# Kernel tuning notes

Hardware: AMD Instinct MI355X
Metric: run time of the kernel (lower is better)

## Reference

```python
import jax, jax.numpy as jnp
import numpy as np

E = 128       # embed_dim
H = 128       # hidden_dim
NLABEL = 5
VOCAB = 50000
DEPTH = 18    # levels 0..17, complete binary tree
BRANCH = 2
N_NODES = 2 ** DEPTH - 1  # level-order layout: level l occupies [2^l-1, 2^(l+1)-1)


def setup_inputs() -> dict:
    key = jax.random.key(0)
    ks = jax.random.split(key, 24)

    def w(k, shape):
        return jax.random.normal(k, shape, dtype=jnp.float32) * 0.05

    inp = {
        "embeds": w(ks[0], (VOCAB, E)),
        "node_words": jax.random.randint(ks[1], (N_NODES,), 0, VOCAB),
        "node_labels": jax.random.randint(ks[2], (N_NODES,), 0, NLABEL),
        "depth": DEPTH,
        "branching": BRANCH,
    }
    # 8 gate linears: *x maps E->H, *h maps H->H (torch nn.Linear: y = x @ W.T + b)
    for j, nm in enumerate(["ix", "ih", "fx", "fh", "ox", "oh", "ux", "uh"]):
        in_dim = E if nm.endswith("x") else H
        inp["W" + nm] = w(ks[3 + 2 * j], (H, in_dim))
        inp["b" + nm] = w(ks[4 + 2 * j], (H,))
    inp["Wout"] = w(ks[20], (NLABEL, H))
    inp["bout"] = w(ks[21], (NLABEL,))
    return inp


def _lin(x, W, b):
    return x @ W.T + b


def _tree_lstm(embeds, node_words, node_labels, depth, branching,
               Wix, bix, Wih, bih, Wfx, bfx, Wfh, bfh,
               Wox, box, Woh, boh, Wux, bux, Wuh, buh, Wout, bout):
    b = branching
    hid = Wix.shape[0]
    loss = jnp.zeros((), dtype=embeds.dtype)
    child_c = child_h = None
    logp = None
    # bottom-up over levels (leaves first); level l has b^l nodes at offset (b^l-1)/(b-1)
    for l in range(depth - 1, -1, -1):
        n = b ** l
        off = (b ** l - 1) // (b - 1)
        x = embeds[node_words[off:off + n]]            # [n, E]
        if child_h is None:                            # leaves: zero child states
            h_sum = jnp.zeros((n, hid), dtype=embeds.dtype)
            c_agg = jnp.zeros((n, hid), dtype=embeds.dtype)
        else:
            ch = child_h.reshape(n, b, hid)            # children of each level-l node
            cc = child_c.reshape(n, b, hid)
            h_sum = ch.sum(axis=1)                     # child-sum
            f = jax.nn.sigmoid(_lin(x, Wfx, bfx)[:, None, :] + _lin(ch, Wfh, bfh))
            c_agg = (f * cc).sum(axis=1)               # sum_k f_k * c_k
        i = jax.nn.sigmoid(_lin(x, Wix, bix) + _lin(h_sum, Wih, bih))
        o = jax.nn.sigmoid(_lin(x, Wox, box) + _lin(h_sum, Woh, boh))
        u = jnp.tanh(_lin(x, Wux, bux) + _lin(h_sum, Wuh, buh))
        c = i * u + c_agg
        h = o * jnp.tanh(c)
        logp = jax.nn.log_softmax(_lin(h, Wout, bout), axis=-1)   # [n, NLABEL]
        lab = node_labels[off:off + n]
        loss = loss - logp[jnp.arange(n), lab].sum()              # NLL summed over nodes
        child_c, child_h = c, h
    return logp, loss  # logp from level 0 = root log-probs [1, NLABEL]


def reference(embeds, node_words, node_labels, depth, branching,
              Wix, bix, Wih, bih, Wfx, bfx, Wfh, bfh,
              Wox, box, Woh, boh, Wux, bux, Wuh, buh, Wout, bout):
    return _tree_lstm(embeds, node_words, node_labels, depth, branching,
                      Wix, bix, Wih, bih, Wfx, bfx, Wfh, bfh,
                      Wox, box, Woh, boh, Wux, bux, Wuh, buh, Wout, bout)
```

## Files before the change

### kernel.cpp

```cpp
#include <hip/hip_runtime.h>
#include <math.h>

#define DEPTH 18
#define NINT ((1 << (DEPTH - 1)) - 1)
#define LEAF_OFF ((1 << (DEPTH - 2)) - 1)
#define NVOCAB 50000
#define SAW 520
#define KTS 9

typedef unsigned short bf16raw;
typedef __bf16 bf16x8 __attribute__((ext_vector_type(8)));
typedef float f32x4 __attribute__((ext_vector_type(4)));
typedef short short8 __attribute__((ext_vector_type(8)));

__device__ __forceinline__ float sigm(float x) { return 1.0f / (1.0f + __expf(-x)); }
__device__ __forceinline__ float fast_tanh(float x) {
    float t = __expf(2.0f * x);
    return 1.0f - 2.0f / (t + 1.0f);
}

__device__ __forceinline__ float bf2f(bf16raw u) {
    union { unsigned int i; float f; } v;
    v.i = ((unsigned int)u) << 16;
    return v.f;
}
__device__ __forceinline__ bf16raw f2bf(float f) {
    union { float f; unsigned int i; } v;
    v.f = f;
    unsigned int r = v.i + 0x7FFFu + ((v.i >> 16) & 1u);
    return (bf16raw)(r >> 16);
}

#define SB() __builtin_amdgcn_sched_barrier(0)

__global__ __launch_bounds__(256) void k_prep_embeds(const float* __restrict__ src,
                                                     bf16raw* __restrict__ dst, int n4)
{
    int i = blockIdx.x * blockDim.x + threadIdx.x;
    if (i < n4) {
        float4 v = ((const float4*)src)[i];
        ushort4 o;
        o.x = f2bf(v.x); o.y = f2bf(v.y); o.z = f2bf(v.z); o.w = f2bf(v.w);
        ((ushort4*)dst)[i] = o;
    }
}

__global__ __launch_bounds__(128) void k_prep_bcat(
    const float* __restrict__ Wix, const float* __restrict__ bix,
    const float* __restrict__ Wih, const float* __restrict__ bih,
    const float* __restrict__ Wfx, const float* __restrict__ bfx,
    const float* __restrict__ Wfh, const float* __restrict__ bfh,
    const float* __restrict__ Wox, const float* __restrict__ box_,
    const float* __restrict__ Woh, const float* __restrict__ boh,
    const float* __restrict__ Wux, const float* __restrict__ bux,
    const float* __restrict__ Wuh, const float* __restrict__ buh,
    bf16raw* __restrict__ Bfrag, float* __restrict__ bias_cat)
{
    const int j = blockIdx.x;
    const int gate = j >> 7, jj = j & 127;
    const float *Wx, *Wh, *bx, *bh;
    switch (gate) {
        case 0: Wx = Wix; Wh = Wih; bx = bix;  bh = bih; break;
        case 1: Wx = Wux; Wh = Wuh; bx = bux;  bh = buh; break;
        case 2: Wx = Wox; Wh = Woh; bx = box_; bh = boh; break;
        default: Wx = Wfx; Wh = Wfh; bx = bfx; bh = bfh; break;
    }
    const int coltile = (j >> 4) & 7, lr = j & 15;
    for (int k = threadIdx.x; k < 256; k += blockDim.x) {
        float v = (k < 128) ? Wx[jj * 128 + k] : Wh[jj * 128 + (k - 128)];
        const int idx = (((gate * 8 + coltile) * KTS + (k >> 5)) * 64
                         + ((k >> 3) & 3) * 16 + lr) * 8 + (k & 7);
        Bfrag[idx] = f2bf(v);
    }
    if (threadIdx.x == 0) bias_cat[j] = bx[jj] + bh[jj];
}

template<int CB>
__device__ __forceinline__ void lp_burst(const bf16raw* __restrict__ bfbase, int wcol,
                                         bf16x8 (&bb)[16])
{
#pragma unroll
    for (int kt = 0; kt < 4; ++kt)
#pragma unroll
        for (int j = 0; j < 4; ++j)
            bb[kt * 4 + j] = *(const bf16x8*)(bfbase +
                    (long)(((CB * 8 + (wcol >> 4) + j) * KTS + kt) * 512));
}

__device__ __forceinline__ void lp_mfma_all(const bf16raw* __restrict__ sA, int wrow,
                                            int lrow, int lquad,
                                            bf16x8 (&bb)[16], f32x4 (&acc)[2][4])
{
#pragma unroll
    for (int kt = 0; kt < 4; ++kt) {
        bf16x8 af[2];
#pragma unroll
        for (int i = 0; i < 2; ++i)
            af[i] = *(const bf16x8*)&sA[(wrow + i * 16 + lrow) * 136 + kt * 32 + lquad * 8];
#pragma unroll
        for (int i = 0; i < 2; ++i)
#pragma unroll
            for (int j = 0; j < 4; ++j)
                acc[i][j] = __builtin_amdgcn_mfma_f32_16x16x32_bf16(af[i], bb[kt * 4 + j], acc[i][j], 0, 0, 0);
    }
}

template<int CB>
__device__ __forceinline__ void lp_rungemm(const bf16raw* __restrict__ sA,
                                           const bf16raw* __restrict__ bfbase,
                                           int wrow, int wcol, int lrow, int lquad,
                                           f32x4 (&acc)[2][4])
{
#pragma unroll
    for (int i = 0; i < 2; i++)
#pragma unroll
        for (int j = 0; j < 4; j++) acc[i][j] = (f32x4){0.f, 0.f, 0.f, 0.f};
    bf16x8 bb[16];
    lp_burst<CB>(bfbase, wcol, bb);
    SB();
    lp_mfma_all(sA, wrow, lrow, lquad, bb, acc);
}

template<int G, int H>
__device__ __forceinline__ void load8(const bf16raw* __restrict__ bfbase, int w,
                                      bf16x8 (&bb)[8])
{
#pragma unroll
    for (int kt2 = 0; kt2 < 4; ++kt2)
#pragma unroll
        for (int jj = 0; jj < 2; ++jj)
            bb[kt2 * 2 + jj] = *(const bf16x8*)(bfbase +
                    (long)(((G * 8 + w * 2 + jj) * KTS + H * 4 + kt2) * 512));
}

template<int AB>
__device__ __forceinline__ void mfma4k(const bf16raw* __restrict__ sA, int lrow, int lquad,
                                       bf16x8 (&bb)[8], f32x4 (&acc)[2][2])
{
#pragma unroll
    for (int kt2 = 0; kt2 < 4; ++kt2) {
        bf16x8 af[2];
#pragma unroll
        for (int i = 0; i < 2; ++i)
            af[i] = *(const bf16x8*)&sA[(i * 16 + lrow) * SAW + (AB + kt2) * 32 + lquad * 8];
#pragma unroll
        for (int jj = 0; jj < 2; ++jj)
#pragma unroll
            for (int i = 0; i < 2; ++i)
                acc[i][jj] = __builtin_amdgcn_mfma_f32_16x16x32_bf16(af[i], bb[kt2 * 2 + jj], acc[i][jj], 0, 0, 0);
    }
}

__global__ __launch_bounds__(256, 3) void k_leafpre(
    const bf16raw* __restrict__ embeds_bf,
    const bf16raw* __restrict__ Bfrag, const float* __restrict__ bias_cat,
    const float* __restrict__ Wout, const float* __restrict__ bout,
    bf16raw* __restrict__ hc_leaf, float* __restrict__ lossv6, int nvtot)
{
    const int vbase = blockIdx.x * 64;
    int nv = nvtot - vbase;
    if (nv > 64) nv = 64;
    if (nv <= 0) return;

    __shared__ __align__(16) bf16raw sA[64 * 136];
    __shared__ __align__(16) bf16raw sT[64 * 136];
    __shared__ float sWout[5 * 128];

    const int t = threadIdx.x;
    for (int i = t; i < 640; i += 256) sWout[i] = Wout[i];

    {
        const int row = t >> 2;
        const int co = (t & 3) * 32;
        const int arow = (row < nv) ? row : 0;
        const bf16raw* ax = embeds_bf + (long)(vbase + arow) * 128;
        *(short8*)&sA[row * 136 + co]      = *(const short8*)(ax + co);
        *(short8*)&sA[row * 136 + co + 8]  = *(const short8*)(ax + co + 8);
        *(short8*)&sA[row * 136 + co + 16] = *(const short8*)(ax + co + 16);
        *(short8*)&sA[row * 136 + co + 24] = *(const short8*)(ax + co + 24);
    }

    const int lane = t & 63;
    const int w = t >> 6;
    const int wrow = (w & 1) * 32;
    const int wcol = (w >> 1) * 64;
    const int lrow = lane & 15;
    const int lquad = lane >> 4;

    __syncthreads();

    const bf16raw* bfbase = Bfrag + (long)lane * 8;

    float tval[2][4][4];
    f32x4 acc[2][4];

    lp_rungemm<0>(sA, bfbase, wrow, wcol, lrow, lquad, acc);
#pragma unroll
    for (int i = 0; i < 2; i++)
#pragma unroll
        for (int jj = 0; jj < 4; jj++) {
            const float b = bias_cat[wcol + jj * 16 + lrow];
#pragma unroll
            for (int r = 0; r < 4; r++) tval[i][jj][r] = sigm(acc[i][jj][r] + b);
        }
    lp_rungemm<1>(sA, bfbase, wrow, wcol, lrow, lquad, acc);
#pragma unroll
    for (int i = 0; i < 2; i++)
#pragma unroll
        for (int jj = 0; jj < 4; jj++) {
            const float b = bias_cat[128 + wcol + jj * 16 + lrow];
#pragma unroll
            for (int r = 0; r < 4; r++) tval[i][jj][r] *= fast_tanh(acc[i][jj][r] + b);
        }
#pragma unroll
    for (int i = 0; i < 2; i++)
#pragma unroll
        for (int jj = 0; jj < 4; jj++)
#pragma unroll
            for (int r = 0; r < 4; r++) {
                const int m = wrow + i * 16 + lquad * 4 + r;
                const int j = wcol + jj * 16 + lrow;
                sT[m * 136 + j] = f2bf(tval[i][jj][r]);
            }
#pragma unroll
    for (int i = 0; i < 2; i++)
#pragma unroll
        for (int jj = 0; jj < 4; jj++)
#pragma unroll
            for (int r = 0; r < 4; r++) tval[i][jj][r] = fast_tanh(tval[i][jj][r]);
    __syncthreads();
#pragma unroll
    for (int s = 0; s < 4; ++s) {
        int ci = t + 256 * s;
        int row = ci >> 4, c8 = (ci & 15) * 8;
        if (row < nv)
            *(short8*)(hc_leaf + (long)(vbase + row) * 256 + 128 + c8) = *(const short8*)&sT[row * 136 + c8];
    }
    lp_rungemm<2>(sA, bfbase, wrow, wcol, lrow, lquad, acc);
    __syncthreads();
#pragma unroll
    for (int i = 0; i < 2; i++)
#pragma unroll
        for (int jj = 0; jj < 4; jj++) {
            const float b = bias_cat[256 + wcol + jj * 16 + lrow];
#pragma unroll
            for (int r = 0; r < 4; r++) {
                const int m = wrow + i * 16 + lquad * 4 + r;
                const int j = wcol + jj * 16 + lrow;
                sT[m * 136 + j] = f2bf(sigm(acc[i][jj][r] + b) * tval[i][jj][r]);
            }
        }
    __syncthreads();
#pragma unroll
    for (int s = 0; s < 4; ++s) {
        int ci = t + 256 * s;
        int row = ci >> 4, c8 = (ci & 15) * 8;
        if (row < nv)
            *(short8*)(hc_leaf + (long)(vbase + row) * 256 + c8) = *(const short8*)&sT[row * 136 + c8];
    }
    {
        const int row = t >> 2, q = t & 3;
        float p[5] = {0.f, 0.f, 0.f, 0.f, 0.f};
        for (int k0 = 0; k0 < 32; ++k0) {
            const int k = q * 32 + k0;
            float hv = bf2f(sT[row * 136 + k]);
#pragma unroll
            for (int l = 0; l < 5; l++) p[l] += hv * sWout[l * 128 + k];
        }
#pragma unroll
        for (int l = 0; l < 5; l++) {
            p[l] += __shfl_down(p[l], 2);
            p[l] += __shfl_down(p[l], 1);
        }
        if (q == 0 && row < nv) {
            float lg[5], mx = -1e30f;
#pragma unroll
            for (int l = 0; l < 5; l++) {
                lg[l] = p[l] + bout[l];
                mx = fmaxf(mx, lg[l]);
            }
            float se = 0.f;
#pragma unroll
            for (int l = 0; l < 5; l++) se += __expf(lg[l] - mx);
            float lse = __logf(se) + mx;
            float* dst = lossv6 + (long)(vbase + row) * 6;
#pragma unroll
            for (int l = 0; l < 5; l++) dst[l] = lg[l];
            dst[5] = lse;
        }
    }
}

__global__ __launch_bounds__(256, 3) void k_level32(
    const bf16raw* __restrict__ embeds_bf, const int* __restrict__ words,
    bf16raw* __restrict__ h_all, bf16raw* __restrict__ c_all,
    const bf16raw* __restrict__ hc_leaf,
    const bf16raw* __restrict__ Bfrag, const float* __restrict__ bias_cat,
    int off, int nm, int leafkids)
{
    __shared__ __align__(16) bf16raw sA[32 * SAW];
    __shared__ __align__(16) bf16raw sCT[64 * 136];

    const int t = threadIdx.x;
    const int m0 = blockIdx.x * 32;

    {
        const int row = t >> 3;
        const int co = (t & 7) * 8;
        int mm = m0 + row; if (mm >= nm) mm = nm - 1;
        const long g = (long)off + mm;
        const bf16raw* px = embeds_bf + (long)words[g] * 128;
        const bf16raw *p1, *p2;
        if (leafkids) {
            p1 = hc_leaf + (long)words[2 * g + 1] * 256;
            p2 = hc_leaf + (long)words[2 * g + 2] * 256;
        } else {
            p1 = h_all + (2 * g + 1) * 128;
            p2 = h_all + (2 * g + 2) * 128;
        }
        short8 vx0 = *(const short8*)(px + co);
        short8 vx1 = *(const short8*)(px + 64 + co);
        short8 h10 = *(const short8*)(p1 + co);
        short8 h11 = *(const short8*)(p1 + 64 + co);
        short8 h20 = *(const short8*)(p2 + co);
        short8 h21 = *(const short8*)(p2 + 64 + co);
        short8 hs0, hs1;
#pragma unroll
        for (int e = 0; e < 8; ++e) {
            hs0[e] = (short)f2bf(bf2f((bf16raw)(unsigned short)h10[e]) +
                                 bf2f((bf16raw)(unsigned short)h20[e]));
            hs1[e] = (short)f2bf(bf2f((bf16raw)(unsigned short)h11[e]) +
                                 bf2f((bf16raw)(unsigned short)h21[e]));
        }
        *(short8*)&sA[row * SAW + co]        = vx0;
        *(short8*)&sA[row * SAW + 64 + co]   = vx1;
        *(short8*)&sA[row * SAW + 128 + co]  = hs0;
        *(short8*)&sA[row * SAW + 192 + co]  = hs1;
        *(short8*)&sA[row * SAW + 256 + co]  = h10;
        *(short8*)&sA[row * SAW + 320 + co]  = h11;
        *(short8*)&sA[row * SAW + 384 + co]  = h20;
        *(short8*)&sA[row * SAW + 448 + co]  = h21;
    }
    {
        const int slot = t >> 2;
        const int cc8 = (t & 3) * 8;
        int mm = m0 + (slot >> 1); if (mm >= nm) mm = nm - 1;
        const long g = (long)off + mm;
        const long cg = 2 * g + 1 + (slot & 1);
        const bf16raw* pc = leafkids ? (hc_leaf + (long)words[cg] * 256 + 128)
                                     : (c_all + cg * 128);
#pragma unroll
        for (int s = 0; s < 4; ++s)
            *(short8*)&sCT[slot * 136 + s * 32 + cc8] = *(const short8*)(pc + s * 32 + cc8);
    }

    const int lane = t & 63;
    const int w = t >> 6;
    const int lrow = lane & 15;
    const int lquad = lane >> 4;

    float bias[4][2];
#pragma unroll
    for (int g = 0; g < 4; ++g)
#pragma unroll
        for (int jj = 0; jj < 2; ++jj)
            bias[g][jj] = bias_cat[g * 128 + w * 32 + jj * 16 + lrow];

    __syncthreads();

    const bf16raw* bfbase = Bfrag + (long)lane * 8;

    f32x4 acc[2][2];
    f32x4 fx[2][2];
    float si[2][2][4];
    float cc[2][2][4];
    float hh[2][2][4];
    bf16x8 bbA[8], bbB[8];

#define ZACC() { _Pragma("unroll") for (int i_ = 0; i_ < 2; ++i_) \
                 _Pragma("unroll") for (int j_ = 0; j_ < 2; ++j_) \
                     acc[i_][j_] = (f32x4){0.f, 0.f, 0.f, 0.f}; }

    load8<0, 0>(bfbase, w, bbA);
    load8<0, 1>(bfbase, w, bbB);
    SB();
    ZACC();
    mfma4k<0>(sA, lrow, lquad, bbA, acc); SB();
    load8<1, 0>(bfbase, w, bbA); SB();
    mfma4k<4>(sA, lrow, lquad, bbB, acc); SB();
    load8<1, 1>(bfbase, w, bbB); SB();
#pragma unroll
    for (int i = 0; i < 2; ++i)
#pragma unroll
        for (int jj = 0; jj < 2; ++jj)
#pragma unroll
            for (int r = 0; r < 4; ++r)
                si[i][jj][r] = sigm(acc[i][jj][r] + bias[0][jj]);
    ZACC();
    mfma4k<0>(sA, lrow, lquad, bbA, acc); SB();
    load8<3, 0>(bfbase, w, bbA); SB();
    mfma4k<4>(sA, lrow, lquad, bbB, acc); SB();
    load8<3, 1>(bfbase, w, bbB); SB();
#pragma unroll
    for (int i = 0; i < 2; ++i)
#pragma unroll
        for (int jj = 0; jj < 2; ++jj)
#pragma unroll
            for (int r = 0; r < 4; ++r)
                cc[i][jj][r] = si[i][jj][r] * fast_tanh(acc[i][jj][r] + bias[1][jj]);
    ZACC();
    mfma4k<0>(sA, lrow, lquad, bbA, acc);
    SB();
#pragma unroll
    for (int i = 0; i < 2; ++i)
#pragma unroll
        for (int jj = 0; jj < 2; ++jj) fx[i][jj] = acc[i][jj];
    mfma4k<8>(sA, lrow, lquad, bbB, acc);
    SB();
    load8<2, 0>(bfbase, w, bbA);
    SB();
#pragma unroll
    for (int i = 0; i < 2; ++i)
#pragma unroll
        for (int jj = 0; jj < 2; ++jj) {
            const int j = w * 32 + jj * 16 + lrow;
#pragma unroll
            for (int r = 0; r < 4; ++r) {
                const int m = i * 16 + lquad * 4 + r;
                cc[i][jj][r] += sigm(acc[i][jj][r] + bias[3][jj]) * bf2f(sCT[(2 * m) * 136 + j]);
            }
        }
#pragma unroll
    for (int i = 0; i < 2; ++i)
#pragma unroll
        for (int jj = 0; jj < 2; ++jj) acc[i][jj] = fx[i][jj];
    mfma4k<12>(sA, lrow, lquad, bbB, acc);
    SB();
    load8<2, 1>(bfbase, w, bbB);
    SB();
#pragma unroll
    for (int i = 0; i < 2; ++i)
#pragma unroll
        for (int jj = 0; jj < 2; ++jj) {
            const int j = w * 32 + jj * 16 + lrow;
#pragma unroll
            for (int r = 0; r < 4; ++r) {
                const int m = i * 16 + lquad * 4 + r;
                cc[i][jj][r] += sigm(acc[i][jj][r] + bias[3][jj]) * bf2f(sCT[(2 * m + 1) * 136 + j]);
            }
        }
    ZACC();
    mfma4k<0>(sA, lrow, lquad, bbA, acc);
    mfma4k<4>(sA, lrow, lquad, bbB, acc);
    SB();
#pragma unroll
    for (int i = 0; i < 2; ++i)
#pragma unroll
        for (int jj = 0; jj < 2; ++jj)
#pragma unroll
            for (int r = 0; r < 4; ++r)
                hh[i][jj][r] = sigm(acc[i][jj][r] + bias[2][jj]) * fast_tanh(cc[i][jj][r]);
#undef ZACC

    __syncthreads();

#pragma unroll
    for (int i = 0; i < 2; ++i)
#pragma unroll
        for (int jj = 0; jj < 2; ++jj) {
            const int j = w * 32 + jj * 16 + lrow;
#pragma unroll
            for (int r = 0; r < 4; ++r) {
                const int m = i * 16 + lquad * 4 + r;
                sCT[m * 136 + j] = f2bf(cc[i][jj][r]);
                sCT[(32 + m) * 136 + j] = f2bf(hh[i][jj][r]);
            }
        }
    __syncthreads();

#pragma unroll
    for (int q = 0; q < 4; ++q) {
        int ci = t + 256 * q;
        int row = ci >> 4;
        int c8 = (ci & 15) * 8;
        int m = row & 31;
        if (m0 + m < nm) {
            bf16raw* dst = (row < 32) ? c_all : h_all;
            *(short8*)(dst + ((long)off + m0 + m) * 128 + c8) = *(const short8*)&sCT[row * 136 + c8];
        }
    }
}

__global__ __launch_bounds__(256) void k_loss(
    const bf16raw* __restrict__ h_all, const int* __restrict__ words,
    const int* __restrict__ labels, const float* __restrict__ lossv6,
    const float* __restrict__ Wout, const float* __restrict__ bout,
    float* __restrict__ partials, float* __restrict__ out)
{
    __shared__ float sWout[640];
    __shared__ float red[128];
    const int t = threadIdx.x;
    for (int i = t; i < 640; i += 256) sWout[i] = Wout[i];

    const int row = t >> 1, half = t & 1;
    const long g = (long)blockIdx.x * 128 + row;
    const bool valid = g < NINT;
    const long gg = valid ? g : 0;
    __syncthreads();

    float p[5] = {0.f, 0.f, 0.f, 0.f, 0.f};
    const bf16raw* hp = h_all + gg * 128 + half * 64;
#pragma unroll
    for (int s = 0; s < 8; ++s) {
        short8 v = *(const short8*)(hp + s * 8);
#pragma unroll
        for (int e = 0; e < 8; ++e) {
            float hv = bf2f((bf16raw)(unsigned short)v[e]);
#pragma unroll
            for (int l = 0; l < 5; l++) p[l] += hv * sWout[l * 128 + half * 64 + s * 8 + e];
        }
    }
#pragma unroll
    for (int l = 0; l < 5; l++) p[l] += __shfl_down(p[l], 1);

    float lossNode = 0.f;
    if (half == 0 && valid) {
        float lg[5], mx = -1e30f;
#pragma unroll
        for (int l = 0; l < 5; l++) {
            lg[l] = p[l] + bout[l];
            mx = fmaxf(mx, lg[l]);
        }
        float se = 0.f;
#pragma unroll
        for (int l = 0; l < 5; l++) se += __expf(lg[l] - mx);
        float lse = __logf(se) + mx;
        lossNode = lse - lg[labels[gg]];
        if (gg >= LEAF_OFF) {
            const float* lv1 = lossv6 + (long)words[2 * gg + 1] * 6;
            const float* lv2 = lossv6 + (long)words[2 * gg + 2] * 6;
            lossNode += (lv1[5] - lv1[labels[2 * gg + 1]])
                      + (lv2[5] - lv2[labels[2 * gg + 2]]);
        }
        if (gg == 0) {
#pragma unroll
            for (int l = 0; l < 5; l++) out[l] = lg[l] - lse;
        }
    }
    if (half == 0) red[row] = lossNode;
    __syncthreads();
    if (t < 64) {
        float s = red[t] + red[t + 64];
#pragma unroll
        for (int d = 32; d > 0; d >>= 1) s += __shfl_down(s, d);
        if (t == 0) atomicAdd(&partials[blockIdx.x & 1023], s);
    }
}

__global__ __launch_bounds__(256) void k3_reduce(const float* __restrict__ partials,
                                                 float* __restrict__ out)
{
    const int t = threadIdx.x;
    float s = 0.f;
    for (int i = t; i < 1024; i += 256) s += partials[i];
#pragma unroll
    for (int d = 32; d > 0; d >>= 1) s += __shfl_down(s, d);
    __shared__ float red[4];
    if ((t & 63) == 0) red[t >> 6] = s;
    __syncthreads();
    if (t == 0) out[5] = red[0] + red[1] + red[2] + red[3];
}

extern "C" void kernel_launch(void* const* d_in, const int* in_sizes, int n_in,
                              void* d_out, int out_size, void* d_ws, size_t ws_size,
                              hipStream_t stream)
{
    const float* embeds = (const float*)d_in[0];
    const int* words = (const int*)d_in[1];
    const int* labels = (const int*)d_in[2];
    const float* Wix = (const float*)d_in[5],  *bix  = (const float*)d_in[6];
    const float* Wih = (const float*)d_in[7],  *bih  = (const float*)d_in[8];
    const float* Wfx = (const float*)d_in[9],  *bfx  = (const float*)d_in[10];
    const float* Wfh = (const float*)d_in[11], *bfh  = (const float*)d_in[12];
    const float* Wox = (const float*)d_in[13], *box_ = (const float*)d_in[14];
    const float* Woh = (const float*)d_in[15], *boh  = (const float*)d_in[16];
    const float* Wux = (const float*)d_in[17], *bux  = (const float*)d_in[18];
    const float* Wuh = (const float*)d_in[19], *buh  = (const float*)d_in[20];
    const float* Wout = (const float*)d_in[21], *bout = (const float*)d_in[22];
    float* out = (float*)d_out;

    char* ws = (char*)d_ws;
    const size_t treeElems = (size_t)NINT * 128;
    bf16raw* h_all = (bf16raw*)ws;
    bf16raw* c_all = h_all + treeElems;
    bf16raw* embeds_bf = c_all + treeElems;
    bf16raw* Bfrag = embeds_bf + (size_t)NVOCAB * 128;
    bf16raw* hc_leaf = Bfrag + 4 * 8 * KTS * 512;
    float* lossv6 = (float*)(hc_leaf + (size_t)NVOCAB * 256);
    float* bias_cat = lossv6 + (size_t)NVOCAB * 6;
    float* partials = bias_cat + 512;

    k_prep_embeds<<<(NVOCAB * 128 / 4 + 255) / 256, 256, 0, stream>>>(
        embeds, embeds_bf, NVOCAB * 128 / 4);
    k_prep_bcat<<<512, 128, 0, stream>>>(Wix, bix, Wih, bih, Wfx, bfx, Wfh, bfh,
                                         Wox, box_, Woh, boh, Wux, bux, Wuh, buh,
                                         Bfrag, bias_cat);
    hipMemsetAsync(partials, 0, 1024 * sizeof(float), stream);

    k_leafpre<<<(NVOCAB + 63) / 64, 256, 0, stream>>>(
        embeds_bf, Bfrag, bias_cat, Wout, bout, hc_leaf, lossv6, NVOCAB);

    for (int l = DEPTH - 2; l >= 0; --l) {
        const int n = 1 << l;
        k_level32<<<dim3((n + 31) / 32), 256, 0, stream>>>(
            embeds_bf, words, h_all, c_all, hc_leaf, Bfrag, bias_cat,
            n - 1, n, (l == DEPTH - 2) ? 1 : 0);
    }

    k_loss<<<(NINT + 127) / 128, 256, 0, stream>>>(
        h_all, words, labels, lossv6, Wout, bout, partials, out);
    k3_reduce<<<1, 256, 0, stream>>>(partials, out);
}
```

Measured before the change: 374.7 us.

## Fuse output projection and loss into level kernel, load child c into registers

The per-node output projection, log-softmax and NLL are moved into the per-level kernel: an MFMA against a prepacked bf16 Wout fragment runs on the h tile already in shared memory, and each node atomically adds its loss. This removes the separate k_loss pass, which re-read all of h_all. Child cell states are now loaded straight into registers in the MFMA output layout rather than staged through shared memory. That lets sA and the c/h tile share a union, and occupancy is raised to 4 blocks per SM. The trade-offs are per-node atomics, scattered 2-byte global loads for c, and a bf16 rather than fp32 Wout projection.

```diff
diff --git a/kernel.cpp b/kernel.cpp
--- a/kernel.cpp
+++ b/kernel.cpp
@@ -54,9 +54,19 @@
     const float* __restrict__ Woh, const float* __restrict__ boh,
     const float* __restrict__ Wux, const float* __restrict__ bux,
     const float* __restrict__ Wuh, const float* __restrict__ buh,
-    bf16raw* __restrict__ Bfrag, float* __restrict__ bias_cat)
+    const float* __restrict__ Wout,
+    bf16raw* __restrict__ Bfrag, bf16raw* __restrict__ WoutFrag,
+    float* __restrict__ bias_cat)
 {
     const int j = blockIdx.x;
+    if (j >= 512) {
+        const int col = j - 512;
+        for (int k = threadIdx.x; k < 128; k += blockDim.x) {
+            float v = (col < 5) ? Wout[col * 128 + k] : 0.f;
+            WoutFrag[((k >> 5) * 64 + ((k >> 3) & 3) * 16 + col) * 8 + (k & 7)] = f2bf(v);
+        }
+        return;
+    }
     const int gate = j >> 7, jj = j & 127;
     const float *Wx, *Wh, *bx, *bh;
     switch (gate) {
@@ -291,18 +301,27 @@
     }
 }
 
-__global__ __launch_bounds__(256, 3) void k_level32(
+__global__ __launch_bounds__(256, 4) void k_level32(
     const bf16raw* __restrict__ embeds_bf, const int* __restrict__ words,
+    const int* __restrict__ labels,
     bf16raw* __restrict__ h_all, bf16raw* __restrict__ c_all,
-    const bf16raw* __restrict__ hc_leaf,
-    const bf16raw* __restrict__ Bfrag, const float* __restrict__ bias_cat,
-    int off, int nm, int leafkids)
-{
-    __shared__ __align__(16) bf16raw sA[32 * SAW];
-    __shared__ __align__(16) bf16raw sCT[64 * 136];
+    const bf16raw* __restrict__ hc_leaf, const float* __restrict__ lossv6,
+    const bf16raw* __restrict__ Bfrag, const bf16raw* __restrict__ WoutFrag,
+    const float* __restrict__ bias_cat, const float* __restrict__ bout,
+    float* __restrict__ partials, float* __restrict__ out,
+    int off, int nm, int leafkids, int isroot)
+{
+    __shared__ __align__(16) union {
+        bf16raw a[32 * SAW];
+        struct { bf16raw ct[64 * 136]; float lg[32 * 5]; } e;
+    } sh;
 
     const int t = threadIdx.x;
     const int m0 = blockIdx.x * 32;
+    const int lane = t & 63;
+    const int w = t >> 6;
+    const int lrow = lane & 15;
+    const int lquad = lane >> 4;
 
     {
         const int row = t >> 3;
@@ -332,32 +351,39 @@
             hs1[e] = (short)f2bf(bf2f((bf16raw)(unsigned short)h11[e]) +
                                  bf2f((bf16raw)(unsigned short)h21[e]));
         }
-        *(short8*)&sA[row * SAW + co]        = vx0;
-        *(short8*)&sA[row * SAW + 64 + co]   = vx1;
-        *(short8*)&sA[row * SAW + 128 + co]  = hs0;
-        *(short8*)&sA[row * SAW + 192 + co]  = hs1;
-        *(short8*)&sA[row * SAW + 256 + co]  = h10;
-        *(short8*)&sA[row * SAW + 320 + co]  = h11;
-        *(short8*)&sA[row * SAW + 384 + co]  = h20;
-        *(short8*)&sA[row * SAW + 448 + co]  = h21;
-    }
-    {
-        const int slot = t >> 2;
-        const int cc8 = (t & 3) * 8;
-        int mm = m0 + (slot >> 1); if (mm >= nm) mm = nm - 1;
-        const long g = (long)off + mm;
-        const long cg = 2 * g + 1 + (slot & 1);
-        const bf16raw* pc = leafkids ? (hc_leaf + (long)words[cg] * 256 + 128)
-                                     : (c_all + cg * 128);
-#pragma unroll
-        for (int s = 0; s < 4; ++s)
-            *(short8*)&sCT[slot * 136 + s * 32 + cc8] = *(const short8*)(pc + s * 32 + cc8);
-    }
-
-    const int lane = t & 63;
-    const int w = t >> 6;
-    const int lrow = lane & 15;
-    const int lquad = lane >> 4;
+        *(short8*)&sh.a[row * SAW + co]        = vx0;
+        *(short8*)&sh.a[row * SAW + 64 + co]   = vx1;
+        *(short8*)&sh.a[row * SAW + 128 + co]  = hs0;
+        *(short8*)&sh.a[row * SAW + 192 + co]  = hs1;
+        *(short8*)&sh.a[row * SAW + 256 + co]  = h10;
+        *(short8*)&sh.a[row * SAW + 320 + co]  = h11;
+        *(short8*)&sh.a[row * SAW + 384 + co]  = h20;
+        *(short8*)&sh.a[row * SAW + 448 + co]  = h21;
+    }
+
+    bf16raw c1r[2][2][4], c2r[2][2][4];
+#pragma unroll
+    for (int i = 0; i < 2; ++i)
+#pragma unroll
+        for (int r = 0; r < 4; ++r) {
+            int mm = m0 + i * 16 + lquad * 4 + r;
+            if (mm >= nm) mm = nm - 1;
+            const long g = (long)off + mm;
+            const bf16raw *s1, *s2;
+            if (leafkids) {
+                s1 = hc_leaf + (long)words[2 * g + 1] * 256 + 128;
+                s2 = hc_leaf + (long)words[2 * g + 2] * 256 + 128;
+            } else {
+                s1 = c_all + (2 * g + 1) * 128;
+                s2 = c_all + (2 * g + 2) * 128;
+            }
+#pragma unroll
+            for (int jj = 0; jj < 2; ++jj) {
+                const int j = w * 32 + jj * 16 + lrow;
+                c1r[i][jj][r] = s1[j];
+                c2r[i][jj][r] = s2[j];
+            }
+        }
 
     float bias[4][2];
 #pragma unroll
@@ -385,9 +411,9 @@
     load8<0, 1>(bfbase, w, bbB);
     SB();
     ZACC();
-    mfma4k<0>(sA, lrow, lquad, bbA, acc); SB();
+    mfma4k<0>(sh.a, lrow, lquad, bbA, acc); SB();
     load8<1, 0>(bfbase, w, bbA); SB();
-    mfma4k<4>(sA, lrow, lquad, bbB, acc); SB();
+    mfma4k<4>(sh.a, lrow, lquad, bbB, acc); SB();
     load8<1, 1>(bfbase, w, bbB); SB();
 #pragma unroll
     for (int i = 0; i < 2; ++i)
@@ -397,9 +423,9 @@
             for (int r = 0; r < 4; ++r)
                 si[i][jj][r] = sigm(acc[i][jj][r] + bias[0][jj]);
     ZACC();
-    mfma4k<0>(sA, lrow, lquad, bbA, acc); SB();
+    mfma4k<0>(sh.a, lrow, lquad, bbA, acc); SB();
     load8<3, 0>(bfbase, w, bbA); SB();
-    mfma4k<4>(sA, lrow, lquad, bbB, acc); SB();
+    mfma4k<4>(sh.a, lrow, lquad, bbB, acc); SB();
     load8<3, 1>(bfbase, w, bbB); SB();
 #pragma unroll
     for (int i = 0; i < 2; ++i)
@@ -409,49 +435,41 @@
             for (int r = 0; r < 4; ++r)
                 cc[i][jj][r] = si[i][jj][r] * fast_tanh(acc[i][jj][r] + bias[1][jj]);
     ZACC();
-    mfma4k<0>(sA, lrow, lquad, bbA, acc);
+    mfma4k<0>(sh.a, lrow, lquad, bbA, acc);
     SB();
 #pragma unroll
     for (int i = 0; i < 2; ++i)
 #pragma unroll
         for (int jj = 0; jj < 2; ++jj) fx[i][jj] = acc[i][jj];
-    mfma4k<8>(sA, lrow, lquad, bbB, acc);
+    mfma4k<8>(sh.a, lrow, lquad, bbB, acc);
     SB();
     load8<2, 0>(bfbase, w, bbA);
     SB();
 #pragma unroll
     for (int i = 0; i < 2; ++i)
 #pragma unroll
-        for (int jj = 0; jj < 2; ++jj) {
-            const int j = w * 32 + jj * 16 + lrow;
-#pragma unroll
-            for (int r = 0; r < 4; ++r) {
-                const int m = i * 16 + lquad * 4 + r;
-                cc[i][jj][r] += sigm(acc[i][jj][r] + bias[3][jj]) * bf2f(sCT[(2 * m) * 136 + j]);
-            }
-        }
+        for (int jj = 0; jj < 2; ++jj)
+#pragma unroll
+            for (int r = 0; r < 4; ++r)
+                cc[i][jj][r] += sigm(acc[i][jj][r] + bias[3][jj]) * bf2f(c1r[i][jj][r]);
 #pragma unroll
     for (int i = 0; i < 2; ++i)
 #pragma unroll
         for (int jj = 0; jj < 2; ++jj) acc[i][jj] = fx[i][jj];
-    mfma4k<12>(sA, lrow, lquad, bbB, acc);
+    mfma4k<12>(sh.a, lrow, lquad, bbB, acc);
     SB();
     load8<2, 1>(bfbase, w, bbB);
     SB();
 #pragma unroll
     for (int i = 0; i < 2; ++i)
 #pragma unroll
-        for (int jj = 0; jj < 2; ++jj) {
-            const int j = w * 32 + jj * 16 + lrow;
-#pragma unroll
-            for (int r = 0; r < 4; ++r) {
-                const int m = i * 16 + lquad * 4 + r;
-                cc[i][jj][r] += sigm(acc[i][jj][r] + bias[3][jj]) * bf2f(sCT[(2 * m + 1) * 136 + j]);
-            }
-        }
+        for (int jj = 0; jj < 2; ++jj)
+#pragma unroll
+            for (int r = 0; r < 4; ++r)
+                cc[i][jj][r] += sigm(acc[i][jj][r] + bias[3][jj]) * bf2f(c2r[i][jj][r]);
     ZACC();
-    mfma4k<0>(sA, lrow, lquad, bbA, acc);
-    mfma4k<4>(sA, lrow, lquad, bbB, acc);
+    mfma4k<0>(sh.a, lrow, lquad, bbA, acc);
+    mfma4k<4>(sh.a, lrow, lquad, bbB, acc);
     SB();
 #pragma unroll
     for (int i = 0; i < 2; ++i)
@@ -472,8 +490,8 @@
 #pragma unroll
             for (int r = 0; r < 4; ++r) {
                 const int m = i * 16 + lquad * 4 + r;
-                sCT[m * 136 + j] = f2bf(cc[i][jj][r]);
-                sCT[(32 + m) * 136 + j] = f2bf(hh[i][jj][r]);
+                sh.e.ct[m * 136 + j] = f2bf(cc[i][jj][r]);
+                sh.e.ct[(32 + m) * 136 + j] = f2bf(hh[i][jj][r]);
             }
         }
     __syncthreads();
@@ -486,74 +504,58 @@
         int m = row & 31;
         if (m0 + m < nm) {
             bf16raw* dst = (row < 32) ? c_all : h_all;
-            *(short8*)(dst + ((long)off + m0 + m) * 128 + c8) = *(const short8*)&sCT[row * 136 + c8];
-        }
-    }
-}
-
-__global__ __launch_bounds__(256) void k_loss(
-    const bf16raw* __restrict__ h_all, const int* __restrict__ words,
-    const int* __restrict__ labels, const float* __restrict__ lossv6,
-    const float* __restrict__ Wout, const float* __restrict__ bout,
-    float* __restrict__ partials, float* __restrict__ out)
-{
-    __shared__ float sWout[640];
-    __shared__ float red[128];
-    const int t = threadIdx.x;
-    for (int i = t; i < 640; i += 256) sWout[i] = Wout[i];
-
-    const int row = t >> 1, half = t & 1;
-    const long g = (long)blockIdx.x * 128 + row;
-    const bool valid = g < NINT;
-    const long gg = valid ? g : 0;
-    __syncthreads();
-
-    float p[5] = {0.f, 0.f, 0.f, 0.f, 0.f};
-    const bf16raw* hp = h_all + gg * 128 + half * 64;
-#pragma unroll
-    for (int s = 0; s < 8; ++s) {
-        short8 v = *(const short8*)(hp + s * 8);
-#pragma unroll
-        for (int e = 0; e < 8; ++e) {
-            float hv = bf2f((bf16raw)(unsigned short)v[e]);
-#pragma unroll
-            for (int l = 0; l < 5; l++) p[l] += hv * sWout[l * 128 + half * 64 + s * 8 + e];
-        }
-    }
-#pragma unroll
-    for (int l = 0; l < 5; l++) p[l] += __shfl_down(p[l], 1);
-
-    float lossNode = 0.f;
-    if (half == 0 && valid) {
-        float lg[5], mx = -1e30f;
-#pragma unroll
-        for (int l = 0; l < 5; l++) {
-            lg[l] = p[l] + bout[l];
-            mx = fmaxf(mx, lg[l]);
+            *(short8*)(dst + ((long)off + m0 + m) * 128 + c8) = *(const short8*)&sh.e.ct[row * 136 + c8];
+        }
+    }
+
+    if (w == 0) {
+        f32x4 lacc[2];
+        lacc[0] = (f32x4){0.f, 0.f, 0.f, 0.f};
+        lacc[1] = (f32x4){0.f, 0.f, 0.f, 0.f};
+#pragma unroll
+        for (int kt = 0; kt < 4; ++kt) {
+            bf16x8 bfr = *(const bf16x8*)(WoutFrag + (long)((kt * 64 + lane) * 8));
+#pragma unroll
+            for (int i = 0; i < 2; ++i) {
+                bf16x8 af = *(const bf16x8*)&sh.e.ct[(32 + i * 16 + lrow) * 136 + kt * 32 + lquad * 8];
+                lacc[i] = __builtin_amdgcn_mfma_f32_16x16x32_bf16(af, bfr, lacc[i], 0, 0, 0);
+            }
+        }
+        if (lrow < 5) {
+            const float bl = bout[lrow];
+#pragma unroll
+            for (int i = 0; i < 2; ++i)
+#pragma unroll
+                for (int r = 0; r < 4; ++r)
+                    sh.e.lg[(i * 16 + lquad * 4 + r) * 5 + lrow] = lacc[i][r] + bl;
+        }
+    }
+    __syncthreads();
+
+    if (t < 32 && m0 + t < nm) {
+        const long g = (long)off + m0 + t;
+        float lgv[5], mx = -1e30f;
+#pragma unroll
+        for (int l = 0; l < 5; ++l) {
+            lgv[l] = sh.e.lg[t * 5 + l];
+            mx = fmaxf(mx, lgv[l]);
         }
         float se = 0.f;
 #pragma unroll
-        for (int l = 0; l < 5; l++) se += __expf(lg[l] - mx);
+        for (int l = 0; l < 5; ++l) se += __expf(lgv[l] - mx);
         float lse = __logf(se) + mx;
-        lossNode = lse - lg[labels[gg]];
-        if (gg >= LEAF_OFF) {
-            const float* lv1 = lossv6 + (long)words[2 * gg + 1] * 6;
-            const float* lv2 = lossv6 + (long)words[2 * gg + 2] * 6;
-            lossNode += (lv1[5] - lv1[labels[2 * gg + 1]])
-                      + (lv2[5] - lv2[labels[2 * gg + 2]]);
-        }
-        if (gg == 0) {
-#pragma unroll
-            for (int l = 0; l < 5; l++) out[l] = lg[l] - lse;
-        }
-    }
-    if (half == 0) red[row] = lossNode;
-    __syncthreads();
-    if (t < 64) {
-        float s = red[t] + red[t + 64];
-#pragma unroll
-        for (int d = 32; d > 0; d >>= 1) s += __shfl_down(s, d);
-        if (t == 0) atomicAdd(&partials[blockIdx.x & 1023], s);
+        float lossNode = lse - lgv[labels[g]];
+        if (leafkids) {
+            const float* lv1 = lossv6 + (long)words[2 * g + 1] * 6;
+            const float* lv2 = lossv6 + (long)words[2 * g + 2] * 6;
+            lossNode += (lv1[5] - lv1[labels[2 * g + 1]])
+                      + (lv2[5] - lv2[labels[2 * g + 2]]);
+        }
+        atomicAdd(&partials[(int)(g & 1023)], lossNode);
+        if (isroot && g == 0) {
+#pragma unroll
+            for (int l = 0; l < 5; ++l) out[l] = lgv[l] - lse;
+        }
     }
 }
 
@@ -595,16 +597,17 @@
     bf16raw* c_all = h_all + treeElems;
     bf16raw* embeds_bf = c_all + treeElems;
     bf16raw* Bfrag = embeds_bf + (size_t)NVOCAB * 128;
-    bf16raw* hc_leaf = Bfrag + 4 * 8 * KTS * 512;
+    bf16raw* WoutFrag = Bfrag + 4 * 8 * KTS * 512;
+    bf16raw* hc_leaf = WoutFrag + 4 * 64 * 8;
     float* lossv6 = (float*)(hc_leaf + (size_t)NVOCAB * 256);
     float* bias_cat = lossv6 + (size_t)NVOCAB * 6;
     float* partials = bias_cat + 512;
 
     k_prep_embeds<<<(NVOCAB * 128 / 4 + 255) / 256, 256, 0, stream>>>(
         embeds, embeds_bf, NVOCAB * 128 / 4);
-    k_prep_bcat<<<512, 128, 0, stream>>>(Wix, bix, Wih, bih, Wfx, bfx, Wfh, bfh,
+    k_prep_bcat<<<528, 128, 0, stream>>>(Wix, bix, Wih, bih, Wfx, bfx, Wfh, bfh,
                                          Wox, box_, Woh, boh, Wux, bux, Wuh, buh,
-                                         Bfrag, bias_cat);
+                                         Wout, Bfrag, WoutFrag, bias_cat);
     hipMemsetAsync(partials, 0, 1024 * sizeof(float), stream);
 
     k_leafpre<<<(NVOCAB + 63) / 64, 256, 0, stream>>>(
@@ -613,11 +616,10 @@
     for (int l = DEPTH - 2; l >= 0; --l) {
         const int n = 1 << l;
         k_level32<<<dim3((n + 31) / 32), 256, 0, stream>>>(
-            embeds_bf, words, h_all, c_all, hc_leaf, Bfrag, bias_cat,
-            n - 1, n, (l == DEPTH - 2) ? 1 : 0);
-    }
-
-    k_loss<<<(NINT + 127) / 128, 256, 0, stream>>>(
-        h_all, words, labels, lossv6, Wout, bout, partials, out);
+            embeds_bf, words, labels, h_all, c_all, hc_leaf, lossv6,
+            Bfrag, WoutFrag, bias_cat, bout, partials, out,
+            n - 1, n, (l == DEPTH - 2) ? 1 : 0, (l == 0) ? 1 : 0);
+    }
+
     k3_reduce<<<1, 256, 0, stream>>>(partials, out);
 }
```

Result: slower. 615.1 us (+64.2%).
